# Kernel tuning notes

Measured on AMD Instinct MI355X. Metric: run time of the kernel, lower is better.

Reference implementation:

```python
import jax, jax.numpy as jnp
import numpy as np

B, S, D, H, O = 128, 512, 128, 1024, 64
IN = 2 * D + 1  # input_size*2 + 1


def _xavier(key, shape):
    fan_out, fan_in = shape
    std = np.sqrt(2.0 / (fan_in + fan_out)).astype(np.float32)
    return jax.random.normal(key, shape, jnp.float32) * std


def setup_inputs() -> dict:
    key = jax.random.key(0)
    ks = jax.random.split(key, 6)
    x = jax.random.normal(ks[0], (B, S, D), jnp.float32)
    mask = jax.random.uniform(ks[1], (B, S, D), jnp.float32)
    ti = jax.random.uniform(ks[2], (B, S, 1), jnp.float32)
    W_ih = _xavier(ks[3], (4 * H, IN))   # LSTMCell weight_ih
    W_hh = _xavier(ks[4], (4 * H, H))    # LSTMCell weight_hh
    b_ih = jnp.zeros((4 * H,), jnp.float32)
    b_hh = jnp.zeros((4 * H,), jnp.float32)
    W_fc = _xavier(ks[5], (O, H))
    b_fc = jnp.zeros((O,), jnp.float32)
    return {"x": x, "mask": mask, "ti": ti, "W_ih": W_ih, "W_hh": W_hh,
            "b_ih": b_ih, "b_hh": b_hh, "W_fc": W_fc, "b_fc": b_fc}


def reference(x, mask, ti, W_ih, W_hh, b_ih, b_hh, W_fc, b_fc):
    b, s, _ = x.shape
    h = W_hh.shape[1]
    xt = jnp.concatenate([x, mask, ti], axis=-1)          # [B,S,IN]
    # Precompute input contribution to gates for all timesteps (one big GEMM)
    xg = jnp.einsum('bsi,gi->sbg', xt, W_ih) + b_ih + b_hh  # [S,B,4H]

    def step(carry, xg_t):
        h_t, c_t = carry
        g = xg_t + h_t @ W_hh.T                             # [B,4H]
        i, f, gg, o = jnp.split(g, 4, axis=-1)              # torch gate order i,f,g,o
        i = jax.nn.sigmoid(i)
        f = jax.nn.sigmoid(f)
        gg = jnp.tanh(gg)
        o = jax.nn.sigmoid(o)
        c_new = f * c_t + i * gg
        h_new = o * jnp.tanh(c_new)
        return (h_new, c_new), None

    h0 = jnp.zeros((b, h), x.dtype)
    c0 = jnp.zeros((b, h), x.dtype)
    (h_last, _), _ = jax.lax.scan(step, (h0, c0), xg)
    return h_last @ W_fc.T + b_fc                           # [B,O]
```

## Files before the change

### kernel.cpp

```cpp
#include <hip/hip_runtime.h>
#include <hip/hip_bf16.h>

typedef __bf16 bf16x8 __attribute__((ext_vector_type(8)));
typedef float f32x4 __attribute__((ext_vector_type(4)));
typedef float f32x2 __attribute__((ext_vector_type(2)));
typedef unsigned int u32x4 __attribute__((ext_vector_type(4)));

#define BB   128
#define SS   512
#define DD   128
#define HH   1024
#define OO   64
#define IIN  257

#define NGROUP 4
#define GBLK   64
#define MG     32
#define KK_H   32
#define KK_X   9

#define XTP_MT    (KK_X*512)
#define HBUF_SLAB (2*KK_H*512)
#define WIH_BLK   (4*KK_X*512)
#define RS        132

#define WS_HBUF  1024
#define WS_HLAST 525312
#define WS_XTP   1049600
#define WS_WIHP  38798336

__device__ __forceinline__ u32x4 ldg_dev16(const void* p) {
  u32x4 r;
  asm volatile("global_load_dwordx4 %0, %1, off sc1" : "=v"(r) : "v"(p));
  return r;
}
__device__ __forceinline__ void stg_dev4(void* p, unsigned int v) {
  asm volatile("global_store_dword %0, %1, off sc1" :: "v"(p), "v"(v));
}
__device__ __forceinline__ bf16x8 asbf(u32x4 v) {
  union { u32x4 u; bf16x8 h; } c; c.u = v; return c.h;
}

#define CLAIMW(CNTSTR, A)                                            \
  asm volatile("s_waitcnt vmcnt(" CNTSTR ")"                         \
    : "+v"((A)[0]), "+v"((A)[1]), "+v"((A)[2]), "+v"((A)[3]),        \
      "+v"((A)[4]), "+v"((A)[5]), "+v"((A)[6]), "+v"((A)[7]))

__global__ void prepack_kernel(const float* __restrict__ x, const float* __restrict__ mask,
                               const float* __restrict__ ti, __bf16* __restrict__ xtp) {
  int idx = blockIdx.x * 256 + threadIdx.x;
  int j = idx & 7, l = (idx >> 3) & 63;
  int rest = idx >> 9;
  int kk = rest % 9;
  int rest2 = rest / 9;
  int mt = rest2 & 1;
  int rest3 = rest2 >> 1;
  int p = rest3 & 3;
  int t = rest3 >> 2;
  int b = p * MG + mt * 16 + (l & 15);
  int k = kk * 32 + ((l >> 4) << 3) + j;
  float v;
  if (k < 128)       v = x[(b * SS + t) * DD + k];
  else if (k < 256)  v = mask[(b * SS + t) * DD + (k - 128)];
  else if (k == 256) v = ti[b * SS + t];
  else               v = 0.f;
  xtp[idx] = (__bf16)v;
}

__global__ void wih_prepack(const float* __restrict__ W_ih, __bf16* __restrict__ wihp) {
  int idx = blockIdx.x * 256 + threadIdx.x;
  int j = idx & 7, l = (idx >> 3) & 63;
  int rest = idx >> 9;
  int kk = rest % 9;
  int rest2 = rest / 9;
  int nt = rest2 & 3, q = rest2 >> 2;
  int col = nt * HH + q * 16 + (l & 15);
  int k = kk * 32 + ((l >> 4) << 3) + j;
  wihp[idx] = (k < IIN) ? (__bf16)W_ih[col * IIN + k] : (__bf16)0.f;
}

__device__ __forceinline__ float sigmoid_f(float v) { return 1.f / (1.f + __expf(-v)); }
__device__ __forceinline__ float tanh_f(float v)    { return 1.f - 2.f / (__expf(2.f * v) + 1.f); }

__launch_bounds__(256, 1)
__global__ void lstm_scan(const float* __restrict__ W_hh,
                          const float* __restrict__ b_ih, const float* __restrict__ b_hh,
                          const __bf16* __restrict__ xtp, const __bf16* __restrict__ wihp,
                          __bf16* __restrict__ hbuf,
                          float* __restrict__ hlast, unsigned int* __restrict__ flags) {
  __shared__ float red_lds[4 * 16 * RS];

  const int tid = threadIdx.x;
  const int bid = blockIdx.x;
  const int p = (bid & 7) >> 1;
  const int q = (bid >> 3) * 2 + (bid & 1);
  const int j0 = q * 16;

  const int w = tid >> 6, l = tid & 63;
  const int n16 = l & 15, qh = l >> 4;
  unsigned int* gflags = flags + p * 64;

  bf16x8 breg[4][8];
  #pragma unroll
  for (int ntI = 0; ntI < 4; ++ntI) {
    const float* wrow = W_hh + (size_t)(ntI * HH + j0 + n16) * HH;
    #pragma unroll
    for (int i = 0; i < 8; ++i) {
      const float* src = wrow + (w * 8 + i) * 32 + qh * 8;
      bf16x8 bv;
      #pragma unroll
      for (int jj = 0; jj < 8; ++jj) bv[jj] = (__bf16)src[jj];
      breg[ntI][i] = bv;
    }
  }

  const int gm = tid >> 3, clp = tid & 7;
  float bias_r[4][2];
  #pragma unroll
  for (int g = 0; g < 4; ++g)
    #pragma unroll
    for (int s = 0; s < 2; ++s) {
      int col = g * HH + j0 + clp * 2 + s;
      bias_r[g][s] = b_ih[col] + b_hh[col];
    }
  float creg[2] = {0.f, 0.f};

  const int xs = (w == 0) ? 0 : (2 * w + 1);
  const int xe = xs + ((w == 0) ? 3 : 2);

  for (int t = 0; t < SS; ++t) {
    const int rb = t & 1, wb = rb ^ 1;
    f32x4 acc[2][4];
    #pragma unroll
    for (int mt = 0; mt < 2; ++mt)
      #pragma unroll
      for (int ntI = 0; ntI < 4; ++ntI) acc[mt][ntI] = (f32x4){0.f, 0.f, 0.f, 0.f};

    for (int kk = xs; kk < xe; ++kk) {
      #pragma unroll
      for (int mt = 0; mt < 2; ++mt) {
        const __bf16* xb = xtp + ((size_t)((t * 4 + p) * 2 + mt)) * XTP_MT + kk * 512 + l * 8;
        bf16x8 a = *(const bf16x8*)xb;
        #pragma unroll
        for (int ntI = 0; ntI < 4; ++ntI) {
          bf16x8 b = *(const bf16x8*)(wihp + ((size_t)(q * 4 + ntI) * 9 + kk) * 512 + l * 8);
          acc[mt][ntI] = __builtin_amdgcn_mfma_f32_16x16x32_bf16(a, b, acc[mt][ntI], 0, 0, 0);
        }
      }
    }

    if (t > 0) {
      if (tid < 64) {
        const unsigned int tgt = (unsigned int)t;
        for (;;) {
          unsigned int fa;
          asm volatile("global_load_dword %0, %1, off sc1\n\t"
                       "s_waitcnt vmcnt(0)"
                       : "=v"(fa) : "v"(gflags + tid));
          if (!__ballot(fa < tgt)) break;
          __builtin_amdgcn_s_sleep(1);
        }
      }
      __syncthreads();
    }

    {
      const __bf16* hbL = hbuf + (p * 2 + rb) * HBUF_SLAB + l * 8;
      u32x4 A0[8], A1[8];
      #pragma unroll
      for (int i = 0; i < 8; ++i) A0[i] = ldg_dev16(hbL + (w * 8 + i) * 512);
      #pragma unroll
      for (int i = 0; i < 8; ++i) A1[i] = ldg_dev16(hbL + (32 + w * 8 + i) * 512);

      CLAIMW("8", A0);
      #pragma unroll
      for (int i = 0; i < 8; ++i)
        #pragma unroll
        for (int ntI = 0; ntI < 4; ++ntI)
          acc[0][ntI] = __builtin_amdgcn_mfma_f32_16x16x32_bf16(asbf(A0[i]), breg[ntI][i], acc[0][ntI], 0, 0, 0);

      CLAIMW("0", A1);
      #pragma unroll
      for (int i = 0; i < 8; ++i)
        #pragma unroll
        for (int ntI = 0; ntI < 4; ++ntI)
          acc[1][ntI] = __builtin_amdgcn_mfma_f32_16x16x32_bf16(asbf(A1[i]), breg[ntI][i], acc[1][ntI], 0, 0, 0);
    }

    #pragma unroll
    for (int mt = 0; mt < 2; ++mt)
      #pragma unroll
      for (int ntI = 0; ntI < 4; ++ntI)
        #pragma unroll
        for (int r = 0; r < 4; ++r)
          red_lds[(ntI * 16 + n16) * RS + (mt * 16 + qh * 4 + r) * 4 + w] = acc[mt][ntI][r];
    __syncthreads();

    {
      __bf16* hw = hbuf + (p * 2 + wb) * HBUF_SLAB;
      float h2[2];
      #pragma unroll
      for (int s = 0; s < 2; ++s) {
        int cl = clp * 2 + s;
        float gv[4];
        #pragma unroll
        for (int g = 0; g < 4; ++g) {
          f32x4 v = *(const f32x4*)(red_lds + (g * 16 + cl) * RS + gm * 4);
          gv[g] = (v[0] + v[1]) + (v[2] + v[3]) + bias_r[g][s];
        }
        float i_ = sigmoid_f(gv[0]);
        float f_ = sigmoid_f(gv[1]);
        float g_ = tanh_f(gv[2]);
        float o_ = sigmoid_f(gv[3]);
        float c  = f_ * creg[s] + i_ * g_;
        creg[s] = c;
        h2[s] = o_ * tanh_f(c);
      }
      union { __bf16 h[2]; unsigned int u; } pk;
      pk.h[0] = (__bf16)h2[0];
      pk.h[1] = (__bf16)h2[1];
      int k = j0 + clp * 2;
      int mt2 = gm >> 4, mm = gm & 15, kk2 = k >> 5, q2 = (k >> 3) & 3, jj = k & 7;
      stg_dev4(hw + ((mt2 * 32 + kk2) * 64 + q2 * 16 + mm) * 8 + jj, pk.u);
      if (t == SS - 1) {
        f32x2 hv = {h2[0], h2[1]};
        *(f32x2*)(hlast + (p * MG + gm) * HH + k) = hv;
      }
    }

    asm volatile("s_waitcnt vmcnt(0)" ::: "memory");
    __syncthreads();
    if (t < SS - 1 && tid == 0) {
      stg_dev4(gflags + q, (unsigned int)(t + 1));
    }
  }
}

__global__ void fc_kernel(const float* __restrict__ hlast, const float* __restrict__ W_fc,
                          const float* __restrict__ b_fc, float* __restrict__ out) {
  int b = blockIdx.x;
  int t = threadIdx.x;
  int o = t >> 2, part = t & 3;
  const float* hr = hlast + b * HH;
  const float* wr = W_fc + o * HH;
  float s = 0.f;
  #pragma unroll 4
  for (int k0 = part * 4; k0 < HH; k0 += 16) {
    float4 hv = *(const float4*)(hr + k0);
    float4 wv = *(const float4*)(wr + k0);
    s += hv.x * wv.x + hv.y * wv.y + hv.z * wv.z + hv.w * wv.w;
  }
  s += __shfl_xor(s, 1);
  s += __shfl_xor(s, 2);
  if (part == 0) out[b * OO + o] = s + b_fc[o];
}

extern "C" void kernel_launch(void* const* d_in, const int* in_sizes, int n_in,
                              void* d_out, int out_size, void* d_ws, size_t ws_size,
                              hipStream_t stream) {
  const float* x    = (const float*)d_in[0];
  const float* mask = (const float*)d_in[1];
  const float* ti   = (const float*)d_in[2];
  const float* W_ih = (const float*)d_in[3];
  const float* W_hh = (const float*)d_in[4];
  const float* b_ih = (const float*)d_in[5];
  const float* b_hh = (const float*)d_in[6];
  const float* W_fc = (const float*)d_in[7];
  const float* b_fc = (const float*)d_in[8];
  float* out = (float*)d_out;

  char* ws = (char*)d_ws;
  unsigned int* flags = (unsigned int*)ws;
  __bf16* hbuf  = (__bf16*)(ws + WS_HBUF);
  float*  hlast = (float*)(ws + WS_HLAST);
  __bf16* xtp   = (__bf16*)(ws + WS_XTP);
  __bf16* wihp  = (__bf16*)(ws + WS_WIHP);

  hipMemsetAsync(ws, 0, WS_HLAST, stream);

  prepack_kernel<<<(SS * NGROUP * 2 * XTP_MT) / 256, 256, 0, stream>>>(x, mask, ti, xtp);
  wih_prepack<<<(GBLK * WIH_BLK) / 256, 256, 0, stream>>>(W_ih, wihp);
  lstm_scan<<<NGROUP * GBLK, 256, 0, stream>>>(W_hh, b_ih, b_hh, xtp, wihp, hbuf, hlast, flags);
  fc_kernel<<<BB, 256, 0, stream>>>(hlast, W_fc, b_fc, out);
}
```

Baseline: 2.245 ms.

## Split batch into eight 16-row groups with per-wave flags and in-register reduction

Doubles the number of batch groups to 8 with 16 rows each, so the persistent scan grid grows to 512 blocks at two blocks per CU. Each block now does one M-tile per step, which halves its hidden-state loads and MFMA work. The cross-wave reduction now has each wave keep its own accumulator lane and add the other waves' partials read from LDS. The trailing block barrier is removed, and each wave publishes its own progress flag, which the consumer polls with dwordx4 loads. The trade-off is more synchronising blocks, more flag traffic, and the whole grid must stay co-resident for the spin-wait scheme to work.

```diff
diff --git a/kernel.cpp b/kernel.cpp
--- a/kernel.cpp
+++ b/kernel.cpp
@@ -3,7 +3,6 @@
 
 typedef __bf16 bf16x8 __attribute__((ext_vector_type(8)));
 typedef float f32x4 __attribute__((ext_vector_type(4)));
-typedef float f32x2 __attribute__((ext_vector_type(2)));
 typedef unsigned int u32x4 __attribute__((ext_vector_type(4)));
 
 #define BB   128
@@ -13,21 +12,20 @@
 #define OO   64
 #define IIN  257
 
-#define NGROUP 4
+#define NGROUP 8
 #define GBLK   64
-#define MG     32
+#define MG     16
 #define KK_H   32
 #define KK_X   9
 
-#define XTP_MT    (KK_X*512)
-#define HBUF_SLAB (2*KK_H*512)
+#define XTP_TP    (KK_X*512)
+#define HBUF_SLAB (KK_H*512)
 #define WIH_BLK   (4*KK_X*512)
-#define RS        132
-
-#define WS_HBUF  1024
-#define WS_HLAST 525312
-#define WS_XTP   1049600
-#define WS_WIHP  38798336
+
+#define WS_HBUF  8192
+#define WS_HLAST 532480
+#define WS_XTP   1056768
+#define WS_WIHP  38805504
 
 __device__ __forceinline__ u32x4 ldg_dev16(const void* p) {
   u32x4 r;
@@ -41,10 +39,9 @@
   union { u32x4 u; bf16x8 h; } c; c.u = v; return c.h;
 }
 
-#define CLAIMW(CNTSTR, A)                                            \
+#define CLAIMW4(CNTSTR, A, O)                                        \
   asm volatile("s_waitcnt vmcnt(" CNTSTR ")"                         \
-    : "+v"((A)[0]), "+v"((A)[1]), "+v"((A)[2]), "+v"((A)[3]),        \
-      "+v"((A)[4]), "+v"((A)[5]), "+v"((A)[6]), "+v"((A)[7]))
+    : "+v"((A)[(O)]), "+v"((A)[(O)+1]), "+v"((A)[(O)+2]), "+v"((A)[(O)+3]))
 
 __global__ void prepack_kernel(const float* __restrict__ x, const float* __restrict__ mask,
                                const float* __restrict__ ti, __bf16* __restrict__ xtp) {
@@ -53,11 +50,9 @@
   int rest = idx >> 9;
   int kk = rest % 9;
   int rest2 = rest / 9;
-  int mt = rest2 & 1;
-  int rest3 = rest2 >> 1;
-  int p = rest3 & 3;
-  int t = rest3 >> 2;
-  int b = p * MG + mt * 16 + (l & 15);
+  int p = rest2 & 7;
+  int t = rest2 >> 3;
+  int b = p * MG + (l & 15);
   int k = kk * 32 + ((l >> 4) << 3) + j;
   float v;
   if (k < 128)       v = x[(b * SS + t) * DD + k];
@@ -82,23 +77,23 @@
 __device__ __forceinline__ float sigmoid_f(float v) { return 1.f / (1.f + __expf(-v)); }
 __device__ __forceinline__ float tanh_f(float v)    { return 1.f - 2.f / (__expf(2.f * v) + 1.f); }
 
-__launch_bounds__(256, 1)
+__launch_bounds__(256, 2)
 __global__ void lstm_scan(const float* __restrict__ W_hh,
                           const float* __restrict__ b_ih, const float* __restrict__ b_hh,
                           const __bf16* __restrict__ xtp, const __bf16* __restrict__ wihp,
                           __bf16* __restrict__ hbuf,
                           float* __restrict__ hlast, unsigned int* __restrict__ flags) {
-  __shared__ float red_lds[4 * 16 * RS];
+  __shared__ float red_lds[8192];
 
   const int tid = threadIdx.x;
   const int bid = blockIdx.x;
-  const int p = (bid & 7) >> 1;
-  const int q = (bid >> 3) * 2 + (bid & 1);
+  const int p = bid >> 6;
+  const int q = bid & 63;
   const int j0 = q * 16;
 
   const int w = tid >> 6, l = tid & 63;
   const int n16 = l & 15, qh = l >> 4;
-  unsigned int* gflags = flags + p * 64;
+  unsigned int* gflags = flags + p * 256;
 
   bf16x8 breg[4][8];
   #pragma unroll
@@ -114,38 +109,29 @@
     }
   }
 
-  const int gm = tid >> 3, clp = tid & 7;
-  float bias_r[4][2];
+  const int grow = qh * 4 + w;
+  float bias_r[4];
   #pragma unroll
   for (int g = 0; g < 4; ++g)
-    #pragma unroll
-    for (int s = 0; s < 2; ++s) {
-      int col = g * HH + j0 + clp * 2 + s;
-      bias_r[g][s] = b_ih[col] + b_hh[col];
-    }
-  float creg[2] = {0.f, 0.f};
+    bias_r[g] = b_ih[g * HH + j0 + n16] + b_hh[g * HH + j0 + n16];
+  float creg = 0.f;
 
   const int xs = (w == 0) ? 0 : (2 * w + 1);
   const int xe = xs + ((w == 0) ? 3 : 2);
 
   for (int t = 0; t < SS; ++t) {
     const int rb = t & 1, wb = rb ^ 1;
-    f32x4 acc[2][4];
+    f32x4 acc[4];
     #pragma unroll
-    for (int mt = 0; mt < 2; ++mt)
-      #pragma unroll
-      for (int ntI = 0; ntI < 4; ++ntI) acc[mt][ntI] = (f32x4){0.f, 0.f, 0.f, 0.f};
+    for (int ntI = 0; ntI < 4; ++ntI) acc[ntI] = (f32x4){0.f, 0.f, 0.f, 0.f};
 
     for (int kk = xs; kk < xe; ++kk) {
-      #pragma unroll
-      for (int mt = 0; mt < 2; ++mt) {
-        const __bf16* xb = xtp + ((size_t)((t * 4 + p) * 2 + mt)) * XTP_MT + kk * 512 + l * 8;
-        bf16x8 a = *(const bf16x8*)xb;
-        #pragma unroll
-        for (int ntI = 0; ntI < 4; ++ntI) {
-          bf16x8 b = *(const bf16x8*)(wihp + ((size_t)(q * 4 + ntI) * 9 + kk) * 512 + l * 8);
-          acc[mt][ntI] = __builtin_amdgcn_mfma_f32_16x16x32_bf16(a, b, acc[mt][ntI], 0, 0, 0);
-        }
+      const __bf16* xb = xtp + ((size_t)(t * 8 + p) * KK_X + kk) * 512 + l * 8;
+      bf16x8 a = *(const bf16x8*)xb;
+      #pragma unroll
+      for (int ntI = 0; ntI < 4; ++ntI) {
+        bf16x8 b = *(const bf16x8*)(wihp + ((size_t)(q * 4 + ntI) * KK_X + kk) * 512 + l * 8);
+        acc[ntI] = __builtin_amdgcn_mfma_f32_16x16x32_bf16(a, b, acc[ntI], 0, 0, 0);
       }
     }
 
@@ -153,11 +139,11 @@
       if (tid < 64) {
         const unsigned int tgt = (unsigned int)t;
         for (;;) {
-          unsigned int fa;
-          asm volatile("global_load_dword %0, %1, off sc1\n\t"
+          u32x4 f4;
+          asm volatile("global_load_dwordx4 %0, %1, off sc1\n\t"
                        "s_waitcnt vmcnt(0)"
-                       : "=v"(fa) : "v"(gflags + tid));
-          if (!__ballot(fa < tgt)) break;
+                       : "=v"(f4) : "v"(gflags + tid * 4));
+          if (!__ballot(f4[0] < tgt || f4[1] < tgt || f4[2] < tgt || f4[3] < tgt)) break;
           __builtin_amdgcn_s_sleep(1);
         }
       }
@@ -165,73 +151,69 @@
     }
 
     {
-      const __bf16* hbL = hbuf + (p * 2 + rb) * HBUF_SLAB + l * 8;
-      u32x4 A0[8], A1[8];
-      #pragma unroll
-      for (int i = 0; i < 8; ++i) A0[i] = ldg_dev16(hbL + (w * 8 + i) * 512);
-      #pragma unroll
-      for (int i = 0; i < 8; ++i) A1[i] = ldg_dev16(hbL + (32 + w * 8 + i) * 512);
-
-      CLAIMW("8", A0);
-      #pragma unroll
-      for (int i = 0; i < 8; ++i)
+      const __bf16* hbL = hbuf + (p * 2 + rb) * HBUF_SLAB + (w * 8) * 512 + l * 8;
+      u32x4 A[8];
+      #pragma unroll
+      for (int i = 0; i < 8; ++i) A[i] = ldg_dev16(hbL + i * 512);
+
+      CLAIMW4("4", A, 0);
+      #pragma unroll
+      for (int i = 0; i < 4; ++i)
         #pragma unroll
         for (int ntI = 0; ntI < 4; ++ntI)
-          acc[0][ntI] = __builtin_amdgcn_mfma_f32_16x16x32_bf16(asbf(A0[i]), breg[ntI][i], acc[0][ntI], 0, 0, 0);
-
-      CLAIMW("0", A1);
-      #pragma unroll
-      for (int i = 0; i < 8; ++i)
+          acc[ntI] = __builtin_amdgcn_mfma_f32_16x16x32_bf16(asbf(A[i]), breg[ntI][i], acc[ntI], 0, 0, 0);
+      CLAIMW4("0", A, 4);
+      #pragma unroll
+      for (int i = 4; i < 8; ++i)
         #pragma unroll
         for (int ntI = 0; ntI < 4; ++ntI)
-          acc[1][ntI] = __builtin_amdgcn_mfma_f32_16x16x32_bf16(asbf(A1[i]), breg[ntI][i], acc[1][ntI], 0, 0, 0);
+          acc[ntI] = __builtin_amdgcn_mfma_f32_16x16x32_bf16(asbf(A[i]), breg[ntI][i], acc[ntI], 0, 0, 0);
     }
 
     #pragma unroll
-    for (int mt = 0; mt < 2; ++mt)
-      #pragma unroll
-      for (int ntI = 0; ntI < 4; ++ntI)
-        #pragma unroll
-        for (int r = 0; r < 4; ++r)
-          red_lds[(ntI * 16 + n16) * RS + (mt * 16 + qh * 4 + r) * 4 + w] = acc[mt][ntI][r];
+    for (int g = 0; g < 4; ++g)
+      #pragma unroll
+      for (int r = 0; r < 4; ++r)
+        red_lds[(((w * 4 + g) * 4 + r) * 4 + qh) * 32 + n16 * 2 + (qh & 1)] = acc[g][r];
     __syncthreads();
 
     {
       __bf16* hw = hbuf + (p * 2 + wb) * HBUF_SLAB;
-      float h2[2];
-      #pragma unroll
-      for (int s = 0; s < 2; ++s) {
-        int cl = clp * 2 + s;
-        float gv[4];
+      float gv[4];
+      #pragma unroll
+      for (int g = 0; g < 4; ++g) {
+        float own = (w == 0) ? acc[g][0] : (w == 1) ? acc[g][1]
+                  : (w == 2) ? acc[g][2] : acc[g][3];
+        float s = own + bias_r[g];
         #pragma unroll
-        for (int g = 0; g < 4; ++g) {
-          f32x4 v = *(const f32x4*)(red_lds + (g * 16 + cl) * RS + gm * 4);
-          gv[g] = (v[0] + v[1]) + (v[2] + v[3]) + bias_r[g][s];
-        }
-        float i_ = sigmoid_f(gv[0]);
-        float f_ = sigmoid_f(gv[1]);
-        float g_ = tanh_f(gv[2]);
-        float o_ = sigmoid_f(gv[3]);
-        float c  = f_ * creg[s] + i_ * g_;
-        creg[s] = c;
-        h2[s] = o_ * tanh_f(c);
-      }
-      union { __bf16 h[2]; unsigned int u; } pk;
-      pk.h[0] = (__bf16)h2[0];
-      pk.h[1] = (__bf16)h2[1];
-      int k = j0 + clp * 2;
-      int mt2 = gm >> 4, mm = gm & 15, kk2 = k >> 5, q2 = (k >> 3) & 3, jj = k & 7;
-      stg_dev4(hw + ((mt2 * 32 + kk2) * 64 + q2 * 16 + mm) * 8 + jj, pk.u);
-      if (t == SS - 1) {
-        f32x2 hv = {h2[0], h2[1]};
-        *(f32x2*)(hlast + (p * MG + gm) * HH + k) = hv;
-      }
+        for (int wo = 0; wo < 4; ++wo)
+          if (wo != w)
+            s += red_lds[(((wo * 4 + g) * 4 + w) * 4 + qh) * 32 + n16 * 2 + (qh & 1)];
+        gv[g] = s;
+      }
+      float i_ = sigmoid_f(gv[0]);
+      float f_ = sigmoid_f(gv[1]);
+      float g_ = tanh_f(gv[2]);
+      float o_ = sigmoid_f(gv[3]);
+      float c  = f_ * creg + i_ * g_;
+      creg = c;
+      float h  = o_ * tanh_f(c);
+
+      union { __bf16 b; unsigned short u; } cv; cv.b = (__bf16)h;
+      unsigned int hu = (unsigned int)cv.u;
+      unsigned int partner = __shfl_xor(hu, 1);
+      if ((n16 & 1) == 0) {
+        unsigned int dw = hu | (partner << 16);
+        int k = j0 + n16;
+        int kk = k >> 5, q2 = (k >> 3) & 3, jj = k & 7;
+        stg_dev4(hw + kk * 512 + (q2 * 16 + grow) * 8 + jj, dw);
+      }
+      if (t == SS - 1) hlast[(p * MG + grow) * HH + j0 + n16] = h;
     }
 
     asm volatile("s_waitcnt vmcnt(0)" ::: "memory");
-    __syncthreads();
-    if (t < SS - 1 && tid == 0) {
-      stg_dev4(gflags + q, (unsigned int)(t + 1));
+    if (t < SS - 1 && l == 0) {
+      stg_dev4(gflags + q * 4 + w, (unsigned int)(t + 1));
     }
   }
 }
@@ -278,7 +260,7 @@
 
   hipMemsetAsync(ws, 0, WS_HLAST, stream);
 
-  prepack_kernel<<<(SS * NGROUP * 2 * XTP_MT) / 256, 256, 0, stream>>>(x, mask, ti, xtp);
+  prepack_kernel<<<(SS * NGROUP * XTP_TP) / 256, 256, 0, stream>>>(x, mask, ti, xtp);
   wih_prepack<<<(GBLK * WIH_BLK) / 256, 256, 0, stream>>>(W_ih, wihp);
   lstm_scan<<<NGROUP * GBLK, 256, 0, stream>>>(W_hh, b_ih, b_hh, xtp, wihp, hbuf, hlast, flags);
   fc_kernel<<<BB, 256, 0, stream>>>(hlast, W_fc, b_fc, out);
```

After: 2.173 ms. 3.2% less time.
